# Kernel tuning notes

Hardware: AMD Instinct MI355X
Metric: run time of the kernel (lower is better)

The kernel has to match this reference:

```python
import jax, jax.numpy as jnp
import numpy as np

EPS_LN = 1e-6


def _ln(x):
    m = jnp.mean(x, axis=-1, keepdims=True)
    v = jnp.mean((x - m) ** 2, axis=-1, keepdims=True)
    return (x - m) * jax.lax.rsqrt(v + EPS_LN)


def _rope(q, cos, sin):
    # q: [B,S,H,D]; cos/sin: [S, D//2]; rotate interleaved pairs
    q2 = q.reshape(q.shape[:-1] + (-1, 2))
    a, b = q2[..., 0], q2[..., 1]
    c = cos[None, :, None, :]
    s = sin[None, :, None, :]
    return jnp.stack([a * c - b * s, a * s + b * c], axis=-1).reshape(q.shape)


def _attn(q, k, v):
    # q:[B,Sq,H,D] k,v:[B,Sk,H,D] -> [B,Sq,H,D]; flash default scale 1/sqrt(D)
    D = q.shape[-1]
    scores = jnp.einsum('bqhd,bkhd->bhqk', q, k) / jnp.sqrt(jnp.asarray(D, q.dtype))
    p = jax.nn.softmax(scores, axis=-1)
    return jnp.einsum('bhqk,bkhd->bqhd', p, v)


def setup_inputs() -> dict:
    key = jax.random.key(0)
    C, H, S, T, B = 2048, 16, 1024, 256, 4
    Dh = C // H
    F = int(C * 4)
    L, Ly = B * S, B * T
    ks = jax.random.split(key, 24)

    def w(k, shape):
        return (jax.random.normal(k, shape, dtype=jnp.float32) * 0.02)

    # RoPE angle table: positions 0..S-1 with standard inverse frequencies
    inv_freq = 1.0 / (10000.0 ** (np.arange(0, Dh, 2, dtype=np.float32) / Dh))
    freqs = jnp.asarray(np.arange(S, dtype=np.float32)[:, None] * inv_freq[None, :])

    inp = {
        'x': jax.random.normal(ks[0], (L, C), dtype=jnp.float32),
        'y': jax.random.normal(ks[1], (Ly, C), dtype=jnp.float32),
        't': jax.random.normal(ks[2], (L, 6 * C), dtype=jnp.float32),
        'freqs': freqs,
        'scale_shift_table': jax.random.normal(ks[3], (6, C), dtype=jnp.float32) / (C ** 0.5),
        'Wq_s': w(ks[4], (C, C)), 'bq_s': jnp.zeros((C,), jnp.float32),
        'Wk_s': w(ks[5], (C, C)), 'bk_s': jnp.zeros((C,), jnp.float32),
        'Wv_s': w(ks[6], (C, C)), 'bv_s': jnp.zeros((C,), jnp.float32),
        'Wo_s': w(ks[7], (C, C)), 'bo_s': jnp.zeros((C,), jnp.float32),
        'Wq_c': w(ks[8], (C, C)), 'bq_c': jnp.zeros((C,), jnp.float32),
        'Wk_c': w(ks[9], (C, C)), 'bk_c': jnp.zeros((C,), jnp.float32),
        'Wv_c': w(ks[10], (C, C)), 'bv_c': jnp.zeros((C,), jnp.float32),
        'Wo_c': w(ks[11], (C, C)), 'bo_c': jnp.zeros((C,), jnp.float32),
        'W_fc1': w(ks[12], (F, C)), 'b_fc1': jnp.zeros((F,), jnp.float32),
        'W_fc2': w(ks[13], (C, F)), 'b_fc2': jnp.zeros((C,), jnp.float32),
        'seq_len': S,
        'txt_len': T,
    }
    return inp


def reference(x, y, t, freqs, scale_shift_table,
              Wq_s, bq_s, Wk_s, bk_s, Wv_s, bv_s, Wo_s, bo_s,
              Wq_c, bq_c, Wk_c, bk_c, Wv_c, bv_c, Wo_c, bo_c,
              W_fc1, b_fc1, W_fc2, b_fc2, seq_len, txt_len):
    L, C = x.shape
    Dh = 2 * freqs.shape[1]
    H = C // Dh
    B = L // seq_len
    cos, sin = jnp.cos(freqs), jnp.sin(freqs)

    # per-token AdaLN params (B here == total tokens in torch code)
    mods = scale_shift_table[None] + t.reshape(L, 6, C)
    shift_msa, scale_msa, gate_msa, shift_mlp, scale_mlp, gate_mlp = (
        mods[:, i, :] for i in range(6))

    # ---- self attention (AdaLN modulate + RoPE) ----
    xm = _ln(x) * (1.0 + scale_msa) + shift_msa
    q = (xm @ Wq_s.T + bq_s).reshape(B, seq_len, H, Dh)
    k = (xm @ Wk_s.T + bk_s).reshape(B, seq_len, H, Dh)
    v = (xm @ Wv_s.T + bv_s).reshape(B, seq_len, H, Dh)
    q = _rope(q, cos, sin)
    k = _rope(k, cos, sin)
    a = _attn(q, k, v).reshape(L, C)
    x = x + gate_msa * (a @ Wo_s.T + bo_s)

    # ---- cross attention (no norm/modulation/gate, no RoPE) ----
    q = (x @ Wq_c.T + bq_c).reshape(B, seq_len, H, Dh)
    k = (y @ Wk_c.T + bk_c).reshape(B, txt_len, H, Dh)
    v = (y @ Wv_c.T + bv_c).reshape(B, txt_len, H, Dh)
    a = _attn(q, k, v).reshape(L, C)
    x = x + (a @ Wo_c.T + bo_c)

    # ---- MLP with AdaLN modulate + gate ----
    xm = _ln(x) * (1.0 + scale_mlp) + shift_mlp
    h = jax.nn.gelu(xm @ W_fc1.T + b_fc1, approximate=True)
    x = x + gate_mlp * (h @ W_fc2.T + b_fc2)
    return x
```

## Files before the change

kernel.cpp:

```cpp
#include <hip/hip_runtime.h>
#include <stdint.h>

#define C_DIM 2048
#define H_NUM 16
#define DH    128
#define S_LEN 1024
#define T_LEN 256
#define B_SZ  4
#define L_ROWS 4096
#define LY_ROWS 1024
#define F_DIM 8192

typedef __attribute__((ext_vector_type(4))) float f32x4;
typedef __attribute__((ext_vector_type(8))) __bf16 bf16x8;
typedef __attribute__((ext_vector_type(4))) unsigned short us4;
typedef __attribute__((ext_vector_type(8))) unsigned short us8;
typedef unsigned short u16;

__device__ __forceinline__ u16 f2bf(float f) {
  union { float f; uint32_t u; } v; v.f = f;
  uint32_t r = v.u + 0x7FFFu + ((v.u >> 16) & 1u);
  return (u16)(r >> 16);
}
__device__ __forceinline__ float bf2f(u16 h) {
  union { uint32_t u; float f; } v; v.u = ((uint32_t)h) << 16;
  return v.f;
}

typedef __attribute__((address_space(1))) void gvoid;
typedef __attribute__((address_space(3))) void lvoid;
__device__ __forceinline__ void gl_lds16(const void* g, void* l) {
  __builtin_amdgcn_global_load_lds((gvoid*)g, (lvoid*)l, 16, 0, 0);
}

template<int N> __device__ __forceinline__ void wait_vmcnt() {
  if constexpr (N == 0) asm volatile("s_waitcnt vmcnt(0)" ::: "memory");
  else if constexpr (N == 3) asm volatile("s_waitcnt vmcnt(3)" ::: "memory");
  else if constexpr (N == 4) asm volatile("s_waitcnt vmcnt(4)" ::: "memory");
}
__device__ __forceinline__ void barrier_raw() {
  asm volatile("s_barrier" ::: "memory");
}

__global__ void k_cvt(const float* __restrict__ src, u16* __restrict__ dst, int n) {
  int i = (blockIdx.x * blockDim.x + threadIdx.x) * 4;
  int stride = gridDim.x * blockDim.x * 4;
  for (; i < n; i += stride) {
    float4 v = *(const float4*)(src + i);
    us4 o;
    o[0] = f2bf(v.x); o[1] = f2bf(v.y); o[2] = f2bf(v.z); o[3] = f2bf(v.w);
    *(us4*)(dst + i) = o;
  }
}

__global__ __launch_bounds__(256)
void k_modln(const float* __restrict__ x, const float* __restrict__ t,
             const float* __restrict__ tab, u16* __restrict__ out,
             int scale_idx, int shift_idx) {
  int row = blockIdx.x;
  int tid = threadIdx.x;
  const float* xr = x + (size_t)row * C_DIM;
  int c0 = tid * 8;
  float4 a = *(const float4*)(xr + c0);
  float4 b = *(const float4*)(xr + c0 + 4);
  float v[8] = {a.x, a.y, a.z, a.w, b.x, b.y, b.z, b.w};
  float s = 0.f, ss = 0.f;
#pragma unroll
  for (int j = 0; j < 8; ++j) { s += v[j]; ss += v[j] * v[j]; }
#pragma unroll
  for (int m = 1; m < 64; m <<= 1) { s += __shfl_xor(s, m); ss += __shfl_xor(ss, m); }
  __shared__ float red[8];
  int wid = tid >> 6;
  if ((tid & 63) == 0) { red[wid * 2] = s; red[wid * 2 + 1] = ss; }
  __syncthreads();
  s  = red[0] + red[2] + red[4] + red[6];
  ss = red[1] + red[3] + red[5] + red[7];
  float mean = s * (1.f / C_DIM);
  float var  = ss * (1.f / C_DIM) - mean * mean;
  float rstd = rsqrtf(var + 1e-6f);
  const float* trow = t + (size_t)row * (6 * C_DIM);
  const float* tsc = trow + scale_idx * C_DIM + c0;
  const float* tsh = trow + shift_idx * C_DIM + c0;
  const float* gsc = tab + scale_idx * C_DIM + c0;
  const float* gsh = tab + shift_idx * C_DIM + c0;
  us8 o;
#pragma unroll
  for (int j = 0; j < 8; ++j) {
    float scv = 1.f + gsc[j] + tsc[j];
    float shv = gsh[j] + tsh[j];
    o[j] = f2bf((v[j] - mean) * rstd * scv + shv);
  }
  *(us8*)(out + (size_t)row * C_DIM + c0) = o;
}

template<int BN, int EPI>
__global__ __launch_bounds__(512, 2)
void k_gemm2(const u16* __restrict__ A, const u16* __restrict__ W,
             const float* __restrict__ bias0, const float* __restrict__ bias1,
             const float* __restrict__ bias2,
             u16* __restrict__ o0, u16* __restrict__ o1, u16* __restrict__ o2,
             int sec_shift, int out_ld,
             float* __restrict__ outF, const float* __restrict__ resid,
             const float* __restrict__ gate_t, const float* __restrict__ gate_tab,
             int M, int N, int K, int nbx) {
  constexpr int ASZ = 256 * 32;
  constexpr int BSZ = BN * 32;
  constexpr int TSZ = ASZ + BSZ;
  constexpr int NREP = BN / 64;
  constexpr int WNT  = BN / 4;
  constexpr int BCALLS = BN / 128;
  constexpr int CALLS  = 2 + BCALLS;
  __shared__ __align__(16) u16 lds[3 * TSZ];

  int tid = threadIdx.x;
  int nwg = gridDim.x;
  int q8 = nwg >> 3, r8 = nwg & 7;
  int xcd = blockIdx.x & 7, local = blockIdx.x >> 3;
  int wgid = (xcd < r8 ? xcd * (q8 + 1) : r8 * (q8 + 1) + (xcd - r8) * q8) + local;
  int bx = wgid % nbx, by = wgid / nbx;
  int m0 = by * 256, n0 = bx * BN;

  int wid = tid >> 6, lane = tid & 63;
  int wm = wid >> 2, wn = wid & 3;
  int lr = lane & 15, lg = lane >> 4;
  int slotr8 = ((lg ^ (lr & 3) ^ ((lr >> 2) & 3)) & 3) * 8;
  int slotg8 = (((tid & 3) ^ ((tid >> 2) & 3) ^ ((tid >> 4) & 3)) & 3) * 8;
  int rstage = tid >> 2;

  auto stageA = [&](int j, int kst, int so) {
    int row = j * 128 + rstage;
    gl_lds16((const char*)A + ((size_t)(m0 + row) * K + kst + slotg8) * 2,
             (char*)lds + (size_t)so * 2 + j * 8192 + tid * 16);
  };
  auto stageB = [&](int j, int kst, int so) {
    int row = j * 128 + rstage;
    gl_lds16((const char*)W + ((size_t)(n0 + row) * K + kst + slotg8) * 2,
             (char*)lds + (size_t)(so + ASZ) * 2 + j * 8192 + tid * 16);
  };

  f32x4 zero4 = {0.f, 0.f, 0.f, 0.f};
  f32x4 acc[8][NREP];
#pragma unroll
  for (int m = 0; m < 8; ++m)
#pragma unroll
    for (int n = 0; n < NREP; ++n) acc[m][n] = zero4;

  int NT = K >> 5;
  stageA(0, 0, 0); stageB(0, 0, 0); stageA(1, 0, 0);
  if constexpr (BCALLS == 2) stageB(1, 0, 0);
  stageA(0, 32, TSZ); stageB(0, 32, TSZ); stageA(1, 32, TSZ);
  if constexpr (BCALLS == 2) stageB(1, 32, TSZ);
  wait_vmcnt<CALLS>();
  barrier_raw();

  int c = 0;
  for (int t = 0; t < NT; ++t) {
    int c2 = c >= 1 ? c - 1 : 2;
    int curo = c * TSZ, stgo = c2 * TSZ;
    int kst = (t + 2) << 5;
    bool st = (t + 2) < NT;
    const u16* curA = lds + curo;
    const u16* curB = lds + curo + ASZ;

    bf16x8 afr[4], bfr[NREP];
#pragma unroll
    for (int n = 0; n < NREP; ++n)
      bfr[n] = *(const bf16x8*)(curB + (wn * WNT + n * 16 + lr) * 32 + slotr8);
#pragma unroll
    for (int m = 0; m < 4; ++m)
      afr[m] = *(const bf16x8*)(curA + (wm * 128 + m * 16 + lr) * 32 + slotr8);
    if (st) { stageA(0, kst, stgo); stageB(0, kst, stgo); }
    barrier_raw();
    __builtin_amdgcn_s_setprio(1);
#pragma unroll
    for (int m = 0; m < 4; ++m)
#pragma unroll
      for (int n = 0; n < NREP; ++n)
        acc[m][n] = __builtin_amdgcn_mfma_f32_16x16x32_bf16(afr[m], bfr[n], acc[m][n], 0, 0, 0);
    __builtin_amdgcn_s_setprio(0);
    barrier_raw();
#pragma unroll
    for (int m = 0; m < 4; ++m)
      afr[m] = *(const bf16x8*)(curA + (wm * 128 + 64 + m * 16 + lr) * 32 + slotr8);
    if (st) { stageA(1, kst, stgo); if constexpr (BCALLS == 2) stageB(1, kst, stgo); }
    barrier_raw();
    __builtin_amdgcn_s_setprio(1);
#pragma unroll
    for (int m = 0; m < 4; ++m)
#pragma unroll
      for (int n = 0; n < NREP; ++n)
        acc[4 + m][n] = __builtin_amdgcn_mfma_f32_16x16x32_bf16(afr[m], bfr[n], acc[4 + m][n], 0, 0, 0);
    __builtin_amdgcn_s_setprio(0);
    if (t + 1 < NT) {
      if (st) wait_vmcnt<CALLS>(); else wait_vmcnt<0>();
      barrier_raw();
    }
    c = c == 2 ? 0 : c + 1;
  }

#pragma unroll
  for (int mf = 0; mf < 8; ++mf) {
    int row0 = m0 + wm * 128 + mf * 16 + lg * 4;
#pragma unroll
    for (int nf = 0; nf < NREP; ++nf) {
      int col = n0 + wn * WNT + nf * 16 + lr;
      if constexpr (EPI == 0) {
        int sec = col >> sec_shift;
        const float* bp = sec == 0 ? bias0 : (sec == 1 ? bias1 : bias2);
        u16* op = sec == 0 ? o0 : (sec == 1 ? o1 : o2);
        int cs = col & ((1 << sec_shift) - 1);
        float bv = bp[cs];
#pragma unroll
        for (int r = 0; r < 4; ++r)
          op[(size_t)(row0 + r) * out_ld + cs] = f2bf(acc[mf][nf][r] + bv);
      } else if constexpr (EPI == 1) {
        float bv = bias0[col];
#pragma unroll
        for (int r = 0; r < 4; ++r) {
          float val = acc[mf][nf][r] + bv;
          float x3 = val * val * val;
          float g = 0.5f * val * (1.f + tanhf(0.7978845608f * (val + 0.044715f * x3)));
          o0[(size_t)(row0 + r) * out_ld + col] = f2bf(g);
        }
      } else if constexpr (EPI == 2) {
        float bv = bias0[col];
        float gt = gate_tab[col];
#pragma unroll
        for (int r = 0; r < 4; ++r) {
          int row = row0 + r;
          size_t idx = (size_t)row * N + col;
          float g = gt + gate_t[(size_t)row * (6 * C_DIM) + col];
          float o = resid[idx] + g * (acc[mf][nf][r] + bv);
          outF[idx] = o;
          if (o0) o0[idx] = f2bf(o);
        }
      } else {
        float bv = bias0[col];
#pragma unroll
        for (int r = 0; r < 4; ++r) {
          size_t idx = (size_t)(row0 + r) * N + col;
          outF[idx] = resid[idx] + (acc[mf][nf][r] + bv);
        }
      }
    }
  }
}

__global__ void k_rope(u16* __restrict__ q, u16* __restrict__ k,
                       const float* __restrict__ freqs) {
  int idx = blockIdx.x * blockDim.x + threadIdx.x;
  int total = L_ROWS * C_DIM / 8;
  for (; idx < total; idx += gridDim.x * blockDim.x) {
    int e = idx * 8;
    int row = e >> 11;
    int col = e & (C_DIM - 1);
    int s = row & (S_LEN - 1);
    int i0 = (col & (DH - 1)) >> 1;
    float4 fr = *(const float4*)(freqs + s * (DH / 2) + i0);
    float cs[4], sn[4];
    float fv[4] = {fr.x, fr.y, fr.z, fr.w};
#pragma unroll
    for (int j = 0; j < 4; ++j) sincosf(fv[j], &sn[j], &cs[j]);
    us8 qa = *(us8*)(q + e);
    us8 ka = *(us8*)(k + e);
#pragma unroll
    for (int p = 0; p < 4; ++p) {
      float a = bf2f(qa[2 * p]), b = bf2f(qa[2 * p + 1]);
      qa[2 * p]     = f2bf(a * cs[p] - b * sn[p]);
      qa[2 * p + 1] = f2bf(a * sn[p] + b * cs[p]);
      float a2 = bf2f(ka[2 * p]), b2 = bf2f(ka[2 * p + 1]);
      ka[2 * p]     = f2bf(a2 * cs[p] - b2 * sn[p]);
      ka[2 * p + 1] = f2bf(a2 * sn[p] + b2 * cs[p]);
    }
    *(us8*)(q + e) = qa;
    *(us8*)(k + e) = ka;
  }
}

__global__ void k_transpose_v(const u16* __restrict__ v, u16* __restrict__ vt, int Lkv) {
  __shared__ u16 tile[32][33];
  int bh = blockIdx.x, b = bh >> 4, h = bh & 15;
  int k0 = blockIdx.y * 32, d0 = blockIdx.z * 32;
  int tx = threadIdx.x, ty = threadIdx.y;
  const u16* src = v + (size_t)(b * Lkv) * C_DIM + h * DH;
#pragma unroll
  for (int j = 0; j < 32; j += 8)
    tile[ty + j][tx] = src[(size_t)(k0 + ty + j) * C_DIM + d0 + tx];
  __syncthreads();
  u16* dst = vt + (size_t)bh * DH * Lkv;
#pragma unroll
  for (int j = 0; j < 32; j += 8)
    dst[(size_t)(d0 + ty + j) * Lkv + k0 + tx] = tile[tx][ty + j];
}

__global__ __launch_bounds__(256)
void k_flash(const u16* __restrict__ Q, const u16* __restrict__ K,
             const u16* __restrict__ Vt, u16* __restrict__ O,
             int Lq, int Lkv, float scale) {
  __shared__ __align__(16) u16 lK[64 * 128];
  __shared__ __align__(16) u16 lV[128 * 64];
  __shared__ __align__(16) u16 lP[4][16 * 72];
  int bh = blockIdx.x, b = bh >> 4, h = bh & 15;
  int tid = threadIdx.x, wid = tid >> 6, lane = tid & 63;
  int lr = lane & 15, lg = lane >> 4;
  int q0 = blockIdx.y * 64 + wid * 16;
  const u16* Qb = Q + ((size_t)(b * Lq) + q0) * C_DIM + h * DH;
  const u16* Kb = K + (size_t)(b * Lkv) * C_DIM + h * DH;
  const u16* Vb = Vt + (size_t)bh * DH * Lkv;

  bf16x8 qf[4];
#pragma unroll
  for (int ks = 0; ks < 4; ++ks)
    qf[ks] = *(const bf16x8*)(Qb + (size_t)lr * C_DIM + ks * 32 + lg * 8);

  f32x4 zero4 = {0.f, 0.f, 0.f, 0.f};
  f32x4 o[8];
#pragma unroll
  for (int n = 0; n < 8; ++n) o[n] = zero4;
  float mrow[4] = {-3.0e38f, -3.0e38f, -3.0e38f, -3.0e38f};
  float lrow[4] = {0.f, 0.f, 0.f, 0.f};

  int nsteps = Lkv >> 6;
  for (int kt = 0; kt < nsteps; ++kt) {
#pragma unroll
    for (int i = 0; i < 4; ++i) {
      int flat = i * 4096 + tid * 16;
      int key = flat >> 8, inner = flat & 255;
      int ksrc = inner ^ ((key & 7) << 4);
      gl_lds16((const char*)Kb + ((size_t)(kt * 64 + key) * C_DIM) * 2 + ksrc, (char*)lK + flat);
      int d = flat >> 7, keyb = flat & 127;
      int vsrc = keyb ^ ((d & 7) << 4);
      gl_lds16((const char*)Vb + ((size_t)d * Lkv) * 2 + kt * 128 + vsrc, (char*)lV + flat);
    }
    __syncthreads();

    f32x4 sc[4];
#pragma unroll
    for (int c = 0; c < 4; ++c) sc[c] = zero4;
#pragma unroll
    for (int c = 0; c < 4; ++c) {
      int key = c * 16 + lr;
#pragma unroll
      for (int ks = 0; ks < 4; ++ks) {
        int off = (ks * 64 + lg * 16) ^ ((key & 7) << 4);
        bf16x8 kf = *(const bf16x8*)((const char*)lK + key * 256 + off);
        sc[c] = __builtin_amdgcn_mfma_f32_16x16x32_bf16(qf[ks], kf, sc[c], 0, 0, 0);
      }
    }
#pragma unroll
    for (int r = 0; r < 4; ++r) {
      float s0 = sc[0][r] * scale, s1 = sc[1][r] * scale;
      float s2 = sc[2][r] * scale, s3 = sc[3][r] * scale;
      float mx = fmaxf(fmaxf(s0, s1), fmaxf(s2, s3));
#pragma unroll
      for (int m = 1; m < 16; m <<= 1) mx = fmaxf(mx, __shfl_xor(mx, m));
      float mnew = fmaxf(mrow[r], mx);
      float alpha = exp2f((mrow[r] - mnew) * 1.44269504f);
      mrow[r] = mnew;
      float p0 = exp2f((s0 - mnew) * 1.44269504f);
      float p1 = exp2f((s1 - mnew) * 1.44269504f);
      float p2 = exp2f((s2 - mnew) * 1.44269504f);
      float p3 = exp2f((s3 - mnew) * 1.44269504f);
      float psum = p0 + p1 + p2 + p3;
#pragma unroll
      for (int m = 1; m < 16; m <<= 1) psum += __shfl_xor(psum, m);
      lrow[r] = lrow[r] * alpha + psum;
#pragma unroll
      for (int n = 0; n < 8; ++n) o[n][r] *= alpha;
      u16* pr = lP[wid] + (4 * lg + r) * 72;
      pr[lr]      = f2bf(p0);
      pr[16 + lr] = f2bf(p1);
      pr[32 + lr] = f2bf(p2);
      pr[48 + lr] = f2bf(p3);
    }
    asm volatile("s_waitcnt lgkmcnt(0)" ::: "memory");
    __builtin_amdgcn_sched_barrier(0);
#pragma unroll
    for (int half = 0; half < 2; ++half) {
      bf16x8 pf = *(const bf16x8*)(lP[wid] + lr * 72 + half * 32 + lg * 8);
#pragma unroll
      for (int n = 0; n < 8; ++n) {
        int d = n * 16 + lr;
        int off = (half * 64 + lg * 16) ^ ((d & 7) << 4);
        bf16x8 vf = *(const bf16x8*)((const char*)lV + d * 128 + off);
        o[n] = __builtin_amdgcn_mfma_f32_16x16x32_bf16(pf, vf, o[n], 0, 0, 0);
      }
    }
    __syncthreads();
  }

  u16* Ob = O + ((size_t)(b * Lq) + q0) * C_DIM + h * DH;
#pragma unroll
  for (int n = 0; n < 8; ++n) {
    int d = n * 16 + lr;
#pragma unroll
    for (int r = 0; r < 4; ++r) {
      int qr = 4 * lg + r;
      Ob[(size_t)qr * C_DIM + d] = f2bf(o[n][r] / lrow[r]);
    }
  }
}

extern "C" void kernel_launch(void* const* d_in, const int* in_sizes, int n_in,
                              void* d_out, int out_size, void* d_ws, size_t ws_size,
                              hipStream_t stream) {
  const float* x     = (const float*)d_in[0];
  const float* y     = (const float*)d_in[1];
  const float* t     = (const float*)d_in[2];
  const float* freqs = (const float*)d_in[3];
  const float* tab   = (const float*)d_in[4];
  const float* Wq_s = (const float*)d_in[5];
  const float* bq_s = (const float*)d_in[6];
  const float* Wk_s = (const float*)d_in[7];
  const float* bk_s = (const float*)d_in[8];
  const float* Wv_s = (const float*)d_in[9];
  const float* bv_s = (const float*)d_in[10];
  const float* Wo_s = (const float*)d_in[11];
  const float* bo_s = (const float*)d_in[12];
  const float* Wq_c = (const float*)d_in[13];
  const float* bq_c = (const float*)d_in[14];
  const float* Wk_c = (const float*)d_in[15];
  const float* bk_c = (const float*)d_in[16];
  const float* Wv_c = (const float*)d_in[17];
  const float* bv_c = (const float*)d_in[18];
  const float* Wo_c = (const float*)d_in[19];
  const float* bo_c = (const float*)d_in[20];
  const float* W_fc1 = (const float*)d_in[21];
  const float* b_fc1 = (const float*)d_in[22];
  const float* W_fc2 = (const float*)d_in[23];
  const float* b_fc2 = (const float*)d_in[24];

  const size_t SZ_CC  = (size_t)C_DIM * C_DIM * 2;
  const size_t SZ_FC  = (size_t)F_DIM * C_DIM * 2;
  const size_t SZ_LC  = (size_t)L_ROWS * C_DIM * 2;
  const size_t SZ_YC  = (size_t)LY_ROWS * C_DIM * 2;
  char* ws = (char*)d_ws;
  size_t off = 0;
  u16* wq_s = (u16*)(ws + off); off += SZ_CC;
  u16* wk_s = (u16*)(ws + off); off += SZ_CC;
  u16* wv_s = (u16*)(ws + off); off += SZ_CC;
  u16* wo_s = (u16*)(ws + off); off += SZ_CC;
  u16* wq_c = (u16*)(ws + off); off += SZ_CC;
  u16* wk_c = (u16*)(ws + off); off += SZ_CC;
  u16* wv_c = (u16*)(ws + off); off += SZ_CC;
  u16* wo_c = (u16*)(ws + off); off += SZ_CC;
  u16* wfc1 = (u16*)(ws + off); off += SZ_FC;
  u16* wfc2 = (u16*)(ws + off); off += SZ_FC;
  u16* ybf  = (u16*)(ws + off); off += SZ_YC;
  u16* xm   = (u16*)(ws + off); off += SZ_LC;
  u16* qb   = (u16*)(ws + off); off += SZ_LC;
  u16* kb   = (u16*)(ws + off); off += SZ_LC;
  u16* vb   = (u16*)(ws + off); off += SZ_LC;
  u16* ao   = (u16*)(ws + off); off += SZ_LC;
  u16* hbuf = qb;
  float* x1 = (float*)(ws + off); off += (size_t)L_ROWS * C_DIM * 4;
  u16* x1bf = (u16*)(ws + off); off += SZ_LC;
  u16* kc   = (u16*)(ws + off); off += SZ_YC;
  u16* vc   = (u16*)(ws + off); off += SZ_YC;
  u16* vt   = (u16*)(ws + off); off += SZ_LC;
  u16* vtc  = (u16*)(ws + off); off += SZ_YC;
  if (ws_size < off) return;

  auto cvt = [&](const float* s, u16* d, int n) {
    int blocks = (n / 4 + 255) / 256; if (blocks > 4096) blocks = 4096;
    k_cvt<<<blocks, 256, 0, stream>>>(s, d, n);
  };
  cvt(Wq_s, wq_s, C_DIM * C_DIM);
  cvt(Wk_s, wk_s, C_DIM * C_DIM);
  cvt(Wv_s, wv_s, C_DIM * C_DIM);
  cvt(Wo_s, wo_s, C_DIM * C_DIM);
  cvt(Wq_c, wq_c, C_DIM * C_DIM);
  cvt(Wk_c, wk_c, C_DIM * C_DIM);
  cvt(Wv_c, wv_c, C_DIM * C_DIM);
  cvt(Wo_c, wo_c, C_DIM * C_DIM);
  cvt(W_fc1, wfc1, F_DIM * C_DIM);
  cvt(W_fc2, wfc2, F_DIM * C_DIM);
  cvt(y, ybf, LY_ROWS * C_DIM);

  const float ascale = 0.08838834764831845f;

  k_modln<<<L_ROWS, 256, 0, stream>>>(x, t, tab, xm, 1, 0);
  k_gemm2<256, 0><<<24 * 16, 512, 0, stream>>>(
      xm, wq_s, bq_s, bk_s, bv_s, qb, kb, vb, 11, C_DIM,
      nullptr, nullptr, nullptr, nullptr, L_ROWS, 6144, C_DIM, 24);
  k_rope<<<2048, 256, 0, stream>>>(qb, kb, freqs);
  k_transpose_v<<<dim3(B_SZ * H_NUM, S_LEN / 32, DH / 32), dim3(32, 8), 0, stream>>>(vb, vt, S_LEN);
  k_flash<<<dim3(B_SZ * H_NUM, S_LEN / 64), 256, 0, stream>>>(qb, kb, vt, ao, S_LEN, S_LEN, ascale);
  k_gemm2<128, 2><<<16 * 16, 512, 0, stream>>>(
      ao, wo_s, bo_s, nullptr, nullptr, x1bf, nullptr, nullptr, 30, C_DIM,
      x1, x, t + 2 * C_DIM, tab + 2 * C_DIM, L_ROWS, C_DIM, C_DIM, 16);
  k_gemm2<128, 0><<<16 * 16, 512, 0, stream>>>(
      x1bf, wq_c, bq_c, nullptr, nullptr, qb, nullptr, nullptr, 30, C_DIM,
      nullptr, nullptr, nullptr, nullptr, L_ROWS, C_DIM, C_DIM, 16);
  k_gemm2<128, 0><<<32 * 4, 512, 0, stream>>>(
      ybf, wk_c, bk_c, bv_c, bv_c, kc, vc, vc, 11, C_DIM,
      nullptr, nullptr, nullptr, nullptr, LY_ROWS, 4096, C_DIM, 32);
  k_transpose_v<<<dim3(B_SZ * H_NUM, T_LEN / 32, DH / 32), dim3(32, 8), 0, stream>>>(vc, vtc, T_LEN);
  k_flash<<<dim3(B_SZ * H_NUM, S_LEN / 64), 256, 0, stream>>>(qb, kc, vtc, ao, S_LEN, T_LEN, ascale);
  k_gemm2<128, 3><<<16 * 16, 512, 0, stream>>>(
      ao, wo_c, bo_c, nullptr, nullptr, nullptr, nullptr, nullptr, 30, C_DIM,
      x1, x1, nullptr, nullptr, L_ROWS, C_DIM, C_DIM, 16);
  k_modln<<<L_ROWS, 256, 0, stream>>>(x1, t, tab, xm, 4, 3);
  k_gemm2<256, 1><<<32 * 16, 512, 0, stream>>>(
      xm, wfc1, b_fc1, nullptr, nullptr, hbuf, nullptr, nullptr, 30, F_DIM,
      nullptr, nullptr, nullptr, nullptr, L_ROWS, F_DIM, C_DIM, 32);
  k_gemm2<128, 2><<<16 * 16, 512, 0, stream>>>(
      hbuf, wfc2, b_fc2, nullptr, nullptr, nullptr, nullptr, nullptr, 30, C_DIM,
      (float*)d_out, x1, t + 5 * C_DIM, tab + 5 * C_DIM, L_ROWS, C_DIM, F_DIM, 16);
}
```

Baseline: 1.026 ms.

## Rewrite GEMM mainloop with 64-wide K tiles and quadrant-split ping-pong staging

Replaces the 3-stage BK=32 GEMM with a double-buffered BK=64 kernel that stages A and B in halves and interleaves four MFMA quadrants with partial loads. N tile is fixed at 256 and M tile becomes the template parameter, so grids are reshaped for every projection. An explicit lgkmcnt wait plus sched_barrier pins LDS reads before each MFMA burst. The aim is fewer barriers per K step and better overlap of global-to-LDS copies with compute, at the cost of a new swizzle and more fragile vmcnt accounting.

```diff
diff --git a/kernel.cpp b/kernel.cpp
--- a/kernel.cpp
+++ b/kernel.cpp
@@ -35,11 +35,15 @@
 
 template<int N> __device__ __forceinline__ void wait_vmcnt() {
   if constexpr (N == 0) asm volatile("s_waitcnt vmcnt(0)" ::: "memory");
-  else if constexpr (N == 3) asm volatile("s_waitcnt vmcnt(3)" ::: "memory");
-  else if constexpr (N == 4) asm volatile("s_waitcnt vmcnt(4)" ::: "memory");
+  else if constexpr (N == 5) asm volatile("s_waitcnt vmcnt(5)" ::: "memory");
+  else if constexpr (N == 6) asm volatile("s_waitcnt vmcnt(6)" ::: "memory");
 }
 __device__ __forceinline__ void barrier_raw() {
   asm volatile("s_barrier" ::: "memory");
+}
+__device__ __forceinline__ void lgkm0_pin() {
+  asm volatile("s_waitcnt lgkmcnt(0)" ::: "memory");
+  __builtin_amdgcn_sched_barrier(0);
 }
 
 __global__ void k_cvt(const float* __restrict__ src, u16* __restrict__ dst, int n) {
@@ -93,9 +97,9 @@
   *(us8*)(out + (size_t)row * C_DIM + c0) = o;
 }
 
-template<int BN, int EPI>
+template<int BM, int EPI>
 __global__ __launch_bounds__(512, 2)
-void k_gemm2(const u16* __restrict__ A, const u16* __restrict__ W,
+void k_gemm3(const u16* __restrict__ A, const u16* __restrict__ W,
              const float* __restrict__ bias0, const float* __restrict__ bias1,
              const float* __restrict__ bias2,
              u16* __restrict__ o0, u16* __restrict__ o1, u16* __restrict__ o2,
@@ -103,14 +107,14 @@
              float* __restrict__ outF, const float* __restrict__ resid,
              const float* __restrict__ gate_t, const float* __restrict__ gate_tab,
              int M, int N, int K, int nbx) {
-  constexpr int ASZ = 256 * 32;
-  constexpr int BSZ = BN * 32;
-  constexpr int TSZ = ASZ + BSZ;
-  constexpr int NREP = BN / 64;
-  constexpr int WNT  = BN / 4;
-  constexpr int BCALLS = BN / 128;
-  constexpr int CALLS  = 2 + BCALLS;
-  __shared__ __align__(16) u16 lds[3 * TSZ];
+  constexpr int HTA = (BM / 2) * 64;
+  constexpr int HTB = 128 * 64;
+  constexpr int ACALLS = BM / 128;
+  constexpr int QM = BM / 64;
+  constexpr int MFR = BM / 32;
+  constexpr int VMN = 4 + ACALLS;
+  constexpr int BOFF = 4 * HTA;
+  __shared__ __align__(16) u16 lds[BOFF + 4 * HTB];
 
   int tid = threadIdx.x;
   int nwg = gridDim.x;
@@ -118,92 +122,143 @@
   int xcd = blockIdx.x & 7, local = blockIdx.x >> 3;
   int wgid = (xcd < r8 ? xcd * (q8 + 1) : r8 * (q8 + 1) + (xcd - r8) * q8) + local;
   int bx = wgid % nbx, by = wgid / nbx;
-  int m0 = by * 256, n0 = bx * BN;
+  int m0 = by * BM, n0 = bx * 256;
 
   int wid = tid >> 6, lane = tid & 63;
   int wm = wid >> 2, wn = wid & 3;
   int lr = lane & 15, lg = lane >> 4;
-  int slotr8 = ((lg ^ (lr & 3) ^ ((lr >> 2) & 3)) & 3) * 8;
-  int slotg8 = (((tid & 3) ^ ((tid >> 2) & 3) ^ ((tid >> 4) & 3)) & 3) * 8;
-  int rstage = tid >> 2;
-
-  auto stageA = [&](int j, int kst, int so) {
-    int row = j * 128 + rstage;
-    gl_lds16((const char*)A + ((size_t)(m0 + row) * K + kst + slotg8) * 2,
-             (char*)lds + (size_t)so * 2 + j * 8192 + tid * 16);
+  int xorslot = ((lr >> 2) & 3) << 1;
+  int bcol = (wn & 1) * 64;
+
+  int tsw = tid ^ (((tid >> 5) & 1) << 1) ^ (((tid >> 6) & 1) << 2);
+  int srow = tsw >> 3;
+  int scol = (tsw & 7) * 8;
+
+  auto stA = [&](int h, int kt2) {
+    int pt = kt2 & 1;
+    u16* dst = lds + (pt * 2 + h) * HTA + tid * 8;
+#pragma unroll
+    for (int call = 0; call < ACALLS; ++call) {
+      int grow = m0 + h * (BM / 2) + call * 64 + srow;
+      gl_lds16(A + (size_t)grow * K + kt2 * 64 + scol, dst + call * 4096);
+    }
   };
-  auto stageB = [&](int j, int kst, int so) {
-    int row = j * 128 + rstage;
-    gl_lds16((const char*)W + ((size_t)(n0 + row) * K + kst + slotg8) * 2,
-             (char*)lds + (size_t)(so + ASZ) * 2 + j * 8192 + tid * 16);
+  auto stB = [&](int h, int kt2) {
+    int pt = kt2 & 1;
+    u16* dst = lds + BOFF + (pt * 2 + h) * HTB + tid * 8;
+#pragma unroll
+    for (int call = 0; call < 2; ++call) {
+      int grow = n0 + h * 128 + call * 64 + srow;
+      gl_lds16(W + (size_t)grow * K + kt2 * 64 + scol, dst + call * 4096);
+    }
   };
 
   f32x4 zero4 = {0.f, 0.f, 0.f, 0.f};
-  f32x4 acc[8][NREP];
-#pragma unroll
-  for (int m = 0; m < 8; ++m)
-#pragma unroll
-    for (int n = 0; n < NREP; ++n) acc[m][n] = zero4;
-
-  int NT = K >> 5;
-  stageA(0, 0, 0); stageB(0, 0, 0); stageA(1, 0, 0);
-  if constexpr (BCALLS == 2) stageB(1, 0, 0);
-  stageA(0, 32, TSZ); stageB(0, 32, TSZ); stageA(1, 32, TSZ);
-  if constexpr (BCALLS == 2) stageB(1, 32, TSZ);
-  wait_vmcnt<CALLS>();
+  f32x4 acc[MFR][4];
+#pragma unroll
+  for (int m = 0; m < MFR; ++m)
+#pragma unroll
+    for (int n = 0; n < 4; ++n) acc[m][n] = zero4;
+
+  int NT2 = K >> 6;
+  stA(0, 0); stA(1, 0); stB(0, 0); stB(1, 0);
+  stB(0, 1); stB(1, 1); stA(0, 1);
+  wait_vmcnt<VMN>();
   barrier_raw();
 
-  int c = 0;
-  for (int t = 0; t < NT; ++t) {
-    int c2 = c >= 1 ? c - 1 : 2;
-    int curo = c * TSZ, stgo = c2 * TSZ;
-    int kst = (t + 2) << 5;
-    bool st = (t + 2) < NT;
-    const u16* curA = lds + curo;
-    const u16* curB = lds + curo + ASZ;
-
-    bf16x8 afr[4], bfr[NREP];
-#pragma unroll
-    for (int n = 0; n < NREP; ++n)
-      bfr[n] = *(const bf16x8*)(curB + (wn * WNT + n * 16 + lr) * 32 + slotr8);
-#pragma unroll
-    for (int m = 0; m < 4; ++m)
-      afr[m] = *(const bf16x8*)(curA + (wm * 128 + m * 16 + lr) * 32 + slotr8);
-    if (st) { stageA(0, kst, stgo); stageB(0, kst, stgo); }
-    barrier_raw();
+  for (int kt = 0; kt < NT2; ++kt) {
+    int p = kt & 1;
+    const u16* Ah = lds + (p * 2 + wm) * HTA;
+    const u16* Bh = lds + BOFF + (p * 2 + (wn >> 1)) * HTB;
+    bf16x8 aR[QM][2], bR0[2][2], bR1[2][2];
+    bool st1 = (kt + 1) < NT2, st2 = (kt + 2) < NT2;
+
+#pragma unroll
+    for (int m = 0; m < QM; ++m) {
+      int r = m * 16 + lr;
+#pragma unroll
+      for (int kk = 0; kk < 2; ++kk)
+        aR[m][kk] = *(const bf16x8*)(Ah + r * 64 + (((kk << 2) | lg) ^ xorslot) * 8);
+    }
+#pragma unroll
+    for (int n = 0; n < 2; ++n) {
+      int r = bcol + n * 16 + lr;
+#pragma unroll
+      for (int kk = 0; kk < 2; ++kk)
+        bR0[n][kk] = *(const bf16x8*)(Bh + r * 64 + (((kk << 2) | lg) ^ xorslot) * 8);
+    }
+    if (st1) stA(1, kt + 1);
+    lgkm0_pin();
     __builtin_amdgcn_s_setprio(1);
 #pragma unroll
-    for (int m = 0; m < 4; ++m)
-#pragma unroll
-      for (int n = 0; n < NREP; ++n)
-        acc[m][n] = __builtin_amdgcn_mfma_f32_16x16x32_bf16(afr[m], bfr[n], acc[m][n], 0, 0, 0);
+    for (int kk = 0; kk < 2; ++kk)
+#pragma unroll
+      for (int m = 0; m < QM; ++m)
+#pragma unroll
+        for (int n = 0; n < 2; ++n)
+          acc[m][n] = __builtin_amdgcn_mfma_f32_16x16x32_bf16(aR[m][kk], bR0[n][kk], acc[m][n], 0, 0, 0);
     __builtin_amdgcn_s_setprio(0);
     barrier_raw();
-#pragma unroll
-    for (int m = 0; m < 4; ++m)
-      afr[m] = *(const bf16x8*)(curA + (wm * 128 + 64 + m * 16 + lr) * 32 + slotr8);
-    if (st) { stageA(1, kst, stgo); if constexpr (BCALLS == 2) stageB(1, kst, stgo); }
+
+#pragma unroll
+    for (int n = 0; n < 2; ++n) {
+      int r = bcol + 32 + n * 16 + lr;
+#pragma unroll
+      for (int kk = 0; kk < 2; ++kk)
+        bR1[n][kk] = *(const bf16x8*)(Bh + r * 64 + (((kk << 2) | lg) ^ xorslot) * 8);
+    }
+    lgkm0_pin();
+    __builtin_amdgcn_s_setprio(1);
+#pragma unroll
+    for (int kk = 0; kk < 2; ++kk)
+#pragma unroll
+      for (int m = 0; m < QM; ++m)
+#pragma unroll
+        for (int n = 0; n < 2; ++n)
+          acc[m][2 + n] = __builtin_amdgcn_mfma_f32_16x16x32_bf16(aR[m][kk], bR1[n][kk], acc[m][2 + n], 0, 0, 0);
+    __builtin_amdgcn_s_setprio(0);
     barrier_raw();
+
+#pragma unroll
+    for (int m = 0; m < QM; ++m) {
+      int r = (BM / 4) + m * 16 + lr;
+#pragma unroll
+      for (int kk = 0; kk < 2; ++kk)
+        aR[m][kk] = *(const bf16x8*)(Ah + r * 64 + (((kk << 2) | lg) ^ xorslot) * 8);
+    }
+    if (st2) { stB(0, kt + 2); stB(1, kt + 2); }
+    lgkm0_pin();
     __builtin_amdgcn_s_setprio(1);
 #pragma unroll
-    for (int m = 0; m < 4; ++m)
-#pragma unroll
-      for (int n = 0; n < NREP; ++n)
-        acc[4 + m][n] = __builtin_amdgcn_mfma_f32_16x16x32_bf16(afr[m], bfr[n], acc[4 + m][n], 0, 0, 0);
+    for (int kk = 0; kk < 2; ++kk)
+#pragma unroll
+      for (int m = 0; m < QM; ++m)
+#pragma unroll
+        for (int n = 0; n < 2; ++n)
+          acc[QM + m][2 + n] = __builtin_amdgcn_mfma_f32_16x16x32_bf16(aR[m][kk], bR1[n][kk], acc[QM + m][2 + n], 0, 0, 0);
     __builtin_amdgcn_s_setprio(0);
-    if (t + 1 < NT) {
-      if (st) wait_vmcnt<CALLS>(); else wait_vmcnt<0>();
-      barrier_raw();
-    }
-    c = c == 2 ? 0 : c + 1;
-  }
-
-#pragma unroll
-  for (int mf = 0; mf < 8; ++mf) {
-    int row0 = m0 + wm * 128 + mf * 16 + lg * 4;
-#pragma unroll
-    for (int nf = 0; nf < NREP; ++nf) {
-      int col = n0 + wn * WNT + nf * 16 + lr;
+    barrier_raw();
+
+    if (st2) stA(0, kt + 2);
+    __builtin_amdgcn_s_setprio(1);
+#pragma unroll
+    for (int kk = 0; kk < 2; ++kk)
+#pragma unroll
+      for (int m = 0; m < QM; ++m)
+#pragma unroll
+        for (int n = 0; n < 2; ++n)
+          acc[QM + m][n] = __builtin_amdgcn_mfma_f32_16x16x32_bf16(aR[m][kk], bR0[n][kk], acc[QM + m][n], 0, 0, 0);
+    __builtin_amdgcn_s_setprio(0);
+    if (st2) wait_vmcnt<VMN>(); else wait_vmcnt<0>();
+    barrier_raw();
+  }
+
+#pragma unroll
+  for (int mf = 0; mf < MFR; ++mf) {
+    int row0 = m0 + wm * (BM / 2) + mf * 16 + lg * 4;
+#pragma unroll
+    for (int nf = 0; nf < 4; ++nf) {
+      int col = n0 + wn * 64 + nf * 16 + lr;
       if constexpr (EPI == 0) {
         int sec = col >> sec_shift;
         const float* bp = sec == 0 ? bias0 : (sec == 1 ? bias1 : bias2);
@@ -480,31 +535,31 @@
   const float ascale = 0.08838834764831845f;
 
   k_modln<<<L_ROWS, 256, 0, stream>>>(x, t, tab, xm, 1, 0);
-  k_gemm2<256, 0><<<24 * 16, 512, 0, stream>>>(
+  k_gemm3<128, 0><<<32 * 24, 512, 0, stream>>>(
       xm, wq_s, bq_s, bk_s, bv_s, qb, kb, vb, 11, C_DIM,
       nullptr, nullptr, nullptr, nullptr, L_ROWS, 6144, C_DIM, 24);
   k_rope<<<2048, 256, 0, stream>>>(qb, kb, freqs);
   k_transpose_v<<<dim3(B_SZ * H_NUM, S_LEN / 32, DH / 32), dim3(32, 8), 0, stream>>>(vb, vt, S_LEN);
   k_flash<<<dim3(B_SZ * H_NUM, S_LEN / 64), 256, 0, stream>>>(qb, kb, vt, ao, S_LEN, S_LEN, ascale);
-  k_gemm2<128, 2><<<16 * 16, 512, 0, stream>>>(
+  k_gemm3<128, 2><<<32 * 8, 512, 0, stream>>>(
       ao, wo_s, bo_s, nullptr, nullptr, x1bf, nullptr, nullptr, 30, C_DIM,
-      x1, x, t + 2 * C_DIM, tab + 2 * C_DIM, L_ROWS, C_DIM, C_DIM, 16);
-  k_gemm2<128, 0><<<16 * 16, 512, 0, stream>>>(
+      x1, x, t + 2 * C_DIM, tab + 2 * C_DIM, L_ROWS, C_DIM, C_DIM, 8);
+  k_gemm3<128, 0><<<32 * 8, 512, 0, stream>>>(
       x1bf, wq_c, bq_c, nullptr, nullptr, qb, nullptr, nullptr, 30, C_DIM,
-      nullptr, nullptr, nullptr, nullptr, L_ROWS, C_DIM, C_DIM, 16);
-  k_gemm2<128, 0><<<32 * 4, 512, 0, stream>>>(
+      nullptr, nullptr, nullptr, nullptr, L_ROWS, C_DIM, C_DIM, 8);
+  k_gemm3<128, 0><<<8 * 16, 512, 0, stream>>>(
       ybf, wk_c, bk_c, bv_c, bv_c, kc, vc, vc, 11, C_DIM,
-      nullptr, nullptr, nullptr, nullptr, LY_ROWS, 4096, C_DIM, 32);
+      nullptr, nullptr, nullptr, nullptr, LY_ROWS, 4096, C_DIM, 16);
   k_transpose_v<<<dim3(B_SZ * H_NUM, T_LEN / 32, DH / 32), dim3(32, 8), 0, stream>>>(vc, vtc, T_LEN);
   k_flash<<<dim3(B_SZ * H_NUM, S_LEN / 64), 256, 0, stream>>>(qb, kc, vtc, ao, S_LEN, T_LEN, ascale);
-  k_gemm2<128, 3><<<16 * 16, 512, 0, stream>>>(
+  k_gemm3<128, 3><<<32 * 8, 512, 0, stream>>>(
       ao, wo_c, bo_c, nullptr, nullptr, nullptr, nullptr, nullptr, 30, C_DIM,
-      x1, x1, nullptr, nullptr, L_ROWS, C_DIM, C_DIM, 16);
+      x1, x1, nullptr, nullptr, L_ROWS, C_DIM, C_DIM, 8);
   k_modln<<<L_ROWS, 256, 0, stream>>>(x1, t, tab, xm, 4, 3);
-  k_gemm2<256, 1><<<32 * 16, 512, 0, stream>>>(
+  k_gemm3<256, 1><<<16 * 32, 512, 0, stream>>>(
       xm, wfc1, b_fc1, nullptr, nullptr, hbuf, nullptr, nullptr, 30, F_DIM,
       nullptr, nullptr, nullptr, nullptr, L_ROWS, F_DIM, C_DIM, 32);
-  k_gemm2<128, 2><<<16 * 16, 512, 0, stream>>>(
+  k_gemm3<128, 2><<<32 * 8, 512, 0, stream>>>(
       hbuf, wfc2, b_fc2, nullptr, nullptr, nullptr, nullptr, nullptr, 30, C_DIM,
-      (float*)d_out, x1, t + 5 * C_DIM, tab + 5 * C_DIM, L_ROWS, C_DIM, F_DIM, 16);
-}
+      (float*)d_out, x1, t + 5 * C_DIM, tab + 5 * C_DIM, L_ROWS, C_DIM, F_DIM, 8);
+}
```

Result: faster. 947.5 us (-7.6%).
